# Performance work log

Hardware: AMD Instinct MI355X
Metric: run time of the kernel (lower is better)

Reference implementation:

```python
import jax, jax.numpy as jnp
import numpy as np

N_NODES = 100000


def _deg_norm(idx, n):
    # inverse-sqrt degree, zero-degree nodes -> 0 (DGL norm='both' convention)
    deg = jax.ops.segment_sum(jnp.ones(idx.shape, jnp.float32), idx, num_segments=n)
    return jnp.where(deg > 0, jax.lax.rsqrt(jnp.maximum(deg, 1.0)), 0.0)


def graph_conv(x, src, dst, W, b, n):
    # symmetric normalization: D_out^{-1/2} on src, D_in^{-1/2} on dst
    norm_src = _deg_norm(src, n)  # [N]
    norm_dst = _deg_norm(dst, n)  # [N]
    h = (x * norm_src[:, None]) @ W          # apply weight first (in >= out)
    msg = h[src]                              # gather [E, out]
    agg = jax.ops.segment_sum(msg, dst, num_segments=n)  # scatter-add [N, out]
    return agg * norm_dst[:, None] + b


def setup_inputs() -> dict:
    key = jax.random.key(0)
    ks = jax.random.split(key, 6)
    x = jax.random.normal(ks[0], (N_NODES, 128), dtype=jnp.float32)
    edge_index = jax.random.randint(ks[1], (2, 1600000), 0, N_NODES, dtype=jnp.int64)
    W1 = jax.random.normal(ks[2], (128, 64), dtype=jnp.float32) * (1.0 / np.sqrt(128))
    b1 = jnp.zeros((64,), jnp.float32)
    W2 = jax.random.normal(ks[3], (64, 32), dtype=jnp.float32) * (1.0 / np.sqrt(64))
    b2 = jnp.zeros((32,), jnp.float32)
    Wl = jax.random.normal(ks[4], (32, 1), dtype=jnp.float32) * (1.0 / np.sqrt(32))
    bl = jnp.zeros((1,), jnp.float32)
    return {"x": x, "edge_index": edge_index, "W1": W1, "b1": b1,
            "W2": W2, "b2": b2, "Wl": Wl, "bl": bl}


def reference(x, edge_index, W1, b1, W2, b2, Wl, bl):
    src, dst = edge_index[0], edge_index[1]
    n = x.shape[0]
    h = graph_conv(x, src, dst, W1, b1, n)
    h = jax.nn.relu(h)
    # dropout(p=0.5) is identity at inference
    h = graph_conv(h, src, dst, W2, b2, n)
    return h @ Wl + bl  # [N, 1]
```

## Files before the change

kernel.cpp:

```cpp
#include <hip/hip_runtime.h>
#include <hip/hip_fp16.h>


#define WAVE 64
#define NRANGE 8
#define NQUAD 2
#define CB 1024
#define CHK 32
#define RB (CB / CHK)

typedef _Float16 f16x8 __attribute__((ext_vector_type(8)));
typedef float f32x4 __attribute__((ext_vector_type(4)));

__global__ __launch_bounds__(256) void k_cnt(const int* __restrict__ dst,
                                             unsigned* __restrict__ cnt,
                                             int E, int B, int chunkEb,
                                             const float* __restrict__ W1,
                                             const float* __restrict__ W2,
                                             const float* __restrict__ b2,
                                             const float* __restrict__ Wl,
                                             const float* __restrict__ bl,
                                             _Float16* __restrict__ wt,
                                             float* __restrict__ w2l,
                                             float* __restrict__ c0) {
    if (blockIdx.x == CB) {
        int t = threadIdx.x;
        for (int i = 0; i < 32; ++i) {
            int e = i * 256 + t;
            int k = e >> 6, n = e & 63;
            wt[n * 128 + k] = (_Float16)W1[e];
        }
        if (t < 64) {
            float acc = 0.f;
#pragma unroll
            for (int j = 0; j < 32; ++j) acc += W2[t * 32 + j] * Wl[j];
            w2l[t] = acc;
        }
        if (t == 0) {
            float s = 0.f;
#pragma unroll
            for (int j = 0; j < 32; ++j) s += b2[j] * Wl[j];
            *c0 = s + bl[0];
        }
        return;
    }
    __shared__ unsigned lc[NRANGE];
    if (threadIdx.x < NRANGE) lc[threadIdx.x] = 0u;
    __syncthreads();
    const int c = blockIdx.x;
    const int beg = c * chunkEb, end = min(beg + chunkEb, E);
    unsigned pc[NRANGE] = {};
    for (int i = beg + (int)threadIdx.x; i < end; i += 256) {
        int r = dst[i] / B;
#pragma unroll
        for (int rr = 0; rr < NRANGE; ++rr) pc[rr] += (r == rr);
    }
#pragma unroll
    for (int rr = 0; rr < NRANGE; ++rr) {
        unsigned v = pc[rr];
#pragma unroll
        for (int off = 32; off; off >>= 1) v += __shfl_xor((int)v, off);
        if ((threadIdx.x & 63) == 0 && v) atomicAdd(&lc[rr], v);
    }
    __syncthreads();
    if (threadIdx.x < NRANGE) cnt[threadIdx.x * CB + c] = lc[threadIdx.x];
}

__global__ __launch_bounds__(256) void k_scancnt2(const unsigned* __restrict__ cnt,
                                                  unsigned* __restrict__ segBase,
                                                  unsigned* __restrict__ rangeCur,
                                                  int SLOT) {
    __shared__ unsigned s[256];
    const int t = threadIdx.x;
    const int PER = (NRANGE * CB) / 256;
    unsigned loc[PER];
    unsigned sum = 0;
#pragma unroll
    for (int j = 0; j < PER; ++j) { loc[j] = sum; sum += cnt[t * PER + j]; }
    s[t] = sum;
    __syncthreads();
    for (int off = 1; off < 256; off <<= 1) {
        unsigned a = (t >= off) ? s[t - off] : 0u;
        __syncthreads();
        s[t] += a;
        __syncthreads();
    }
    unsigned base = s[t] - sum;
#pragma unroll
    for (int j = 0; j < PER; ++j) segBase[t * PER + j] = base + loc[j];
    if (t == 255) segBase[NRANGE * CB] = s[255];
    if (t < NRANGE) rangeCur[t] = (unsigned)(t * SLOT);
}

__global__ __launch_bounds__(256) void k_hist(const int* __restrict__ srcArr,
                                              const int* __restrict__ dstArr,
                                              unsigned* __restrict__ partial_s,
                                              unsigned* __restrict__ partial_d,
                                              int E, int B, int chunkE) {
    extern __shared__ unsigned hist[];
    const int q = blockIdx.x & (NQUAD - 1);
    const int c = blockIdx.x >> 1;
    const int lo = q * 4 * B;
    const int* nodes = blockIdx.y ? dstArr : srcArr;
    unsigned* partial = blockIdx.y ? partial_d : partial_s;

    for (int b = threadIdx.x; b < B; b += 256) hist[b] = 0u;
    __syncthreads();

    const int beg = c * chunkE, end = min(beg + chunkE, E);
    const int n4 = (end - beg) >> 2;
    const int4* p = (const int4*)(nodes + beg);
    for (int j = threadIdx.x; j < n4; j += 256) {
        int4 v = p[j];
#pragma unroll
        for (int k = 0; k < 4; ++k) {
            int a = (&v.x)[k] - lo;
            if ((unsigned)a < (unsigned)(4 * B)) {
                int h2 = (a >= 2 * B);
                int r2 = a - (h2 ? 2 * B : 0);
                int h1 = (r2 >= B);
                int bin = r2 - (h1 ? B : 0);
                atomicAdd(&hist[bin], 1u << (((h2 << 1) | h1) << 3));
            }
        }
    }
    for (int j = beg + (n4 << 2) + threadIdx.x; j < end; j += 256) {
        int a = nodes[j] - lo;
        if ((unsigned)a < (unsigned)(4 * B)) {
            int h2 = (a >= 2 * B);
            int r2 = a - (h2 ? 2 * B : 0);
            int h1 = (r2 >= B);
            int bin = r2 - (h1 ? B : 0);
            atomicAdd(&hist[bin], 1u << (((h2 << 1) | h1) << 3));
        }
    }
    __syncthreads();
    unsigned* outp = partial + (size_t)(q * CHK + c) * B;
    for (int b = threadIdx.x; b < B; b += 256) outp[b] = hist[b];
}

__global__ __launch_bounds__(256) void k_bucket(const int* __restrict__ src,
                                                const int* __restrict__ dst,
                                                const unsigned* __restrict__ segBase,
                                                unsigned* __restrict__ ebuf,
                                                int E, int B, int chunkEb) {
    __shared__ unsigned lcnt[NRANGE];
    const int c = blockIdx.x;
    const int lane = threadIdx.x & 63;
    if (threadIdx.x < NRANGE) lcnt[threadIdx.x] = 0u;
    __syncthreads();

    unsigned sb[NRANGE];
#pragma unroll
    for (int r = 0; r < NRANGE; ++r) sb[r] = segBase[r * CB + c];

    const int beg = c * chunkEb, end = min(beg + chunkEb, E);
    for (int i = beg + (int)threadIdx.x; i < end; i += 256) {
        int d = dst[i];
        int s = src[i];
        int r = d / B;
        unsigned pk = ((unsigned)(d - r * B) << 17) | (unsigned)s;
#pragma unroll
        for (int rr = 0; rr < NRANGE; ++rr) {
            unsigned long long m = __ballot(r == rr);
            if (m) {
                int leader = __ffsll((long long)m) - 1;
                unsigned base = 0;
                if (lane == leader) base = atomicAdd(&lcnt[rr], (unsigned)__popcll(m));
                base = (unsigned)__shfl((int)base, leader);
                if (r == rr) {
                    unsigned before = (unsigned)__popcll(m & ((1ull << lane) - 1ull));
                    ebuf[sb[rr] + base + before] = pk;
                }
            }
        }
    }
}

__global__ __launch_bounds__(256) void k_reduce_norm(const unsigned* __restrict__ partial_s,
                                                     unsigned* __restrict__ partial_d,
                                                     float* __restrict__ norm_s,
                                                     float* __restrict__ norm_d,
                                                     unsigned* __restrict__ deg_d,
                                                     unsigned* __restrict__ offsets,
                                                     unsigned* __restrict__ rangeCur,
                                                     int N, int B, int Bpad) {
    int t = blockIdx.x * 256 + threadIdx.x;
    int lane = threadIdx.x & 63;
    const int half = NQUAD * Bpad;
    if (t < half) {
        int q = t / Bpad, b = t - q * Bpad;
        bool valid = (b < B);
        unsigned run = 0;
        if (valid) {
            size_t base = (size_t)(q * CHK) * B + b;
            unsigned acc = 0;
            for (int c = 0; c < CHK; ++c) {
                size_t ix = base + (size_t)c * B;
                unsigned v = partial_d[ix];
                partial_d[ix] = acc;
                acc += v;
            }
            run = acc;
        }
#pragma unroll
        for (int j = 0; j < 4; ++j) {
            unsigned d1 = valid ? ((run >> (8 * j)) & 0xffu) : 0u;
            unsigned p = d1;
#pragma unroll
            for (int off = 1; off < 64; off <<= 1) {
                unsigned o = (unsigned)__shfl_up((int)p, off);
                if (lane >= off) p += o;
            }
            unsigned tot = (unsigned)__shfl((int)p, 63);
            int r = q * 4 + j;
            unsigned wbase = 0;
            if (lane == 63 && tot) wbase = atomicAdd(&rangeCur[r], tot);
            wbase = (unsigned)__shfl((int)wbase, 63);
            if (valid) {
                int n = q * 4 * B + j * B + b;
                if (n < N) {
                    deg_d[n] = d1;
                    norm_d[n] = d1 ? rsqrtf((float)d1) : 0.0f;
                    offsets[n] = wbase + (p - d1);
                }
            }
        }
    } else {
        t -= half;
        int q = t / Bpad, b = t - q * Bpad;
        if (q >= NQUAD || b >= B) return;
        size_t base = (size_t)(q * CHK) * B + b;
        unsigned ds = 0;
        for (int c = 0; c < CHK; ++c) ds += partial_s[base + (size_t)c * B];
#pragma unroll
        for (int j = 0; j < 4; ++j) {
            int n = q * 4 * B + j * B + b;
            if (n < N) {
                unsigned d0 = (ds >> (8 * j)) & 0xffu;
                norm_s[n] = d0 ? rsqrtf((float)d0) : 0.0f;
            }
        }
    }
}

__global__ __launch_bounds__(256) void k_fill2(const unsigned* __restrict__ ebuf,
                                               const unsigned* __restrict__ segBase,
                                               const unsigned* __restrict__ offsets,
                                               const unsigned* __restrict__ rel,
                                               unsigned* __restrict__ csr,
                                               int N, int B) {
    extern __shared__ unsigned curs[];
    const int r = blockIdx.x & (NRANGE - 1);
    const int ch = blockIdx.x >> 3;
    const int lo = r * B;
    const int bins = min(B, N - lo);
    const int sh = (r & 3) << 3;
    const unsigned* relp = rel + (size_t)((r >> 2) * CHK + ch) * B;
    for (int b = threadIdx.x; b < bins; b += 256)
        curs[b] = offsets[lo + b] + ((relp[b] >> sh) & 0xffu);
    __syncthreads();

    const unsigned s0 = segBase[r * CB + ch * RB];
    const unsigned s1 = segBase[r * CB + ch * RB + RB];
    for (unsigned i = s0 + threadIdx.x; i < s1; i += 256) {
        unsigned e = ebuf[i];
        unsigned bin = e >> 17;
        if (bin < (unsigned)bins)
            csr[atomicAdd(&curs[bin], 1u)] = e & 0x1ffffu;
    }
}

__global__ __launch_bounds__(256) void k_gemm1(const float* __restrict__ x,
                                               const _Float16* __restrict__ wt,
                                               const float* __restrict__ norm_s,
                                               __half* __restrict__ h1h, int N) {
    __shared__ __align__(16) _Float16 xs[64 * 128];
    const int tid = threadIdx.x, lane = tid & 63, wv = tid >> 6;
    const int r0 = blockIdx.x * 64;

    f16x8 bf[4][4];
#pragma unroll
    for (int kt = 0; kt < 4; ++kt)
#pragma unroll
        for (int nt = 0; nt < 4; ++nt)
            bf[kt][nt] = *(const f16x8*)&wt[(nt * 16 + (lane & 15)) * 128 +
                                            kt * 32 + (lane >> 4) * 8];

#pragma unroll
    for (int it = 0; it < 8; ++it) {
        int e = it * 256 + tid;
        int r = e >> 5, c = e & 31;
        int row = r0 + r;
        float4 v = (row < N) ? ((const float4*)x)[(size_t)row * 32 + c]
                             : make_float4(0.f, 0.f, 0.f, 0.f);
        __half2 lo2 = __floats2half2_rn(v.x, v.y);
        __half2 hi2 = __floats2half2_rn(v.z, v.w);
        uint2 pk;
        pk.x = *(unsigned*)&lo2;
        pk.y = *(unsigned*)&hi2;
        int byte = r * 256 + c * 8;
        byte ^= (r & 7) << 4;
        *(uint2*)((char*)xs + byte) = pk;
    }
    __syncthreads();

    f32x4 acc[4] = {};
    const int rloc = wv * 16 + (lane & 15);
#pragma unroll
    for (int kt = 0; kt < 4; ++kt) {
        int byte = rloc * 256 + (kt * 32 + (lane >> 4) * 8) * 2;
        byte ^= (rloc & 7) << 4;
        f16x8 af = *(const f16x8*)((char*)xs + byte);
#pragma unroll
        for (int nt = 0; nt < 4; ++nt)
            acc[nt] = __builtin_amdgcn_mfma_f32_16x16x32_f16(af, bf[kt][nt], acc[nt], 0, 0, 0);
    }

#pragma unroll
    for (int j = 0; j < 4; ++j) {
        int row = r0 + wv * 16 + (lane >> 4) * 4 + j;
        if (row < N) {
            float ns = norm_s[row];
#pragma unroll
            for (int nt = 0; nt < 4; ++nt)
                h1h[(size_t)row * 64 + nt * 16 + (lane & 15)] =
                    __float2half(acc[nt][j] * ns);
        }
    }
}

__global__ __launch_bounds__(256) void k_agg_rdot(const unsigned* __restrict__ offsets,
                                                  const unsigned* __restrict__ deg_d,
                                                  const unsigned* __restrict__ csr,
                                                  const __half* __restrict__ h1h,
                                                  const float* __restrict__ norm_s,
                                                  const float* __restrict__ norm_d,
                                                  const float* __restrict__ b1,
                                                  const float* __restrict__ w2l,
                                                  float* __restrict__ s_node, int N) {
    const int lane = threadIdx.x & 63;
    const int slot = lane >> 4;
    const int p = lane & 15;
    const int v = (blockIdx.x * 256 + threadIdx.x) >> 6;
    if (v >= N) return;
    const unsigned beg = offsets[v];
    const unsigned end = beg + deg_d[v];

    float a0 = 0.f, a1 = 0.f, a2 = 0.f, a3 = 0.f;
#define GATHER(sreg) { \
        uint2 u = *(const uint2*)&h1h[(size_t)(sreg) * 64 + 4 * p]; \
        float2 f0 = __half22float2(*(__half2*)&u.x); \
        float2 f1 = __half22float2(*(__half2*)&u.y); \
        a0 += f0.x; a1 += f0.y; a2 += f1.x; a3 += f1.y; }

    for (unsigned base = beg; base < end; base += WAVE) {
        const int n = (int)min((unsigned)WAVE, end - base);
        int sv = (lane < n) ? (int)csr[base + lane] : 0;
        int i = 0;
        for (; i + 32 <= n; i += 32) {
            int s0 = __shfl(sv, i + 0 + slot);
            int s1 = __shfl(sv, i + 4 + slot);
            int s2 = __shfl(sv, i + 8 + slot);
            int s3 = __shfl(sv, i + 12 + slot);
            int s4 = __shfl(sv, i + 16 + slot);
            int s5 = __shfl(sv, i + 20 + slot);
            int s6 = __shfl(sv, i + 24 + slot);
            int s7 = __shfl(sv, i + 28 + slot);
            GATHER(s0); GATHER(s1); GATHER(s2); GATHER(s3);
            GATHER(s4); GATHER(s5); GATHER(s6); GATHER(s7);
        }
        for (; i + 16 <= n; i += 16) {
            int s0 = __shfl(sv, i + 0 + slot);
            int s1 = __shfl(sv, i + 4 + slot);
            int s2 = __shfl(sv, i + 8 + slot);
            int s3 = __shfl(sv, i + 12 + slot);
            GATHER(s0); GATHER(s1); GATHER(s2); GATHER(s3);
        }
        for (; i < n; i += 4) {
            int e = i + slot;
            int s = __shfl(sv, min(e, n - 1));
            if (e < n) GATHER(s);
        }
    }
#undef GATHER
    a0 += __shfl_xor(a0, 16); a0 += __shfl_xor(a0, 32);
    a1 += __shfl_xor(a1, 16); a1 += __shfl_xor(a1, 32);
    a2 += __shfl_xor(a2, 16); a2 += __shfl_xor(a2, 32);
    a3 += __shfl_xor(a3, 16); a3 += __shfl_xor(a3, 32);

    float nd = norm_d[v];
    float4 bq = *(const float4*)&b1[4 * p];
    float4 wq = *(const float4*)&w2l[4 * p];
    float t = fmaxf(fmaf(a0, nd, bq.x), 0.f) * wq.x
            + fmaxf(fmaf(a1, nd, bq.y), 0.f) * wq.y
            + fmaxf(fmaf(a2, nd, bq.z), 0.f) * wq.z
            + fmaxf(fmaf(a3, nd, bq.w), 0.f) * wq.w;
#pragma unroll
    for (int off = 8; off; off >>= 1) t += __shfl_xor(t, off);
    if (lane == 0) s_node[v] = t * norm_s[v];
}

__global__ __launch_bounds__(256) void k_out(const unsigned* __restrict__ offsets,
                                             const unsigned* __restrict__ deg_d,
                                             const unsigned* __restrict__ csr,
                                             const float* __restrict__ s_node,
                                             const float* __restrict__ norm_d,
                                             const float* __restrict__ c0,
                                             float* __restrict__ out, int N) {
    int t = blockIdx.x * 256 + threadIdx.x;
    int v = t >> 2, slot = t & 3;
    if (v >= N) return;
    unsigned beg = offsets[v], end = beg + deg_d[v];
    float sum = 0.f;
    for (unsigned j = beg + slot; j < end; j += 4)
        sum += s_node[csr[j]];
    sum += __shfl_xor(sum, 1);
    sum += __shfl_xor(sum, 2);
    if (slot == 0) out[v] = fmaf(sum, norm_d[v], *c0);
}

extern "C" void kernel_launch(void* const* d_in, const int* in_sizes, int n_in,
                              void* d_out, int out_size, void* d_ws, size_t ws_size,
                              hipStream_t stream) {
    const float* x  = (const float*)d_in[0];
    const int*   ei = (const int*)d_in[1];
    const float* W1 = (const float*)d_in[2];
    const float* b1 = (const float*)d_in[3];
    const float* W2 = (const float*)d_in[4];
    const float* b2 = (const float*)d_in[5];
    const float* Wl = (const float*)d_in[6];
    const float* bl = (const float*)d_in[7];

    const int N = in_sizes[0] / 128;
    const int E = in_sizes[1] / 2;
    const int* src = ei;
    const int* dst = ei + E;
    const int B = (N + NRANGE - 1) / NRANGE;
    const int Bpad = ((B + 63) / 64) * 64;
    const int SLOT = E / NRANGE + 16384;
    const int chunkEb = (E + CB - 1) / CB;
    const int chunkE = chunkEb * RB;

    char* w = (char*)d_ws;
    auto alloc = [&](size_t bytes) -> void* {
        void* r = (void*)w;
        w += (bytes + 255) & ~(size_t)255;
        return r;
    };
    float*    norm_s    = (float*)alloc((size_t)N * 4);
    float*    norm_d    = (float*)alloc((size_t)N * 4);
    unsigned* deg_d     = (unsigned*)alloc((size_t)N * 4);
    unsigned* offsets   = (unsigned*)alloc((size_t)N * 4);
    __half*   h1h       = (__half*)alloc((size_t)N * 64 * 2);
    unsigned* csr       = (unsigned*)alloc((size_t)NRANGE * SLOT * 4);
    float*    s_node    = (float*)alloc((size_t)N * 4);
    float*    w2l       = (float*)alloc(64 * 4);
    float*    c0        = (float*)alloc(4);
    _Float16* wt        = (_Float16*)alloc(64 * 128 * 2);
    unsigned* ebuf      = (unsigned*)alloc((size_t)E * 4);
    unsigned* cnt       = (unsigned*)alloc((size_t)(NRANGE * CB + 1) * 4);
    unsigned* segBase   = (unsigned*)alloc((size_t)(NRANGE * CB + 1) * 4);
    unsigned* rangeCur  = (unsigned*)alloc(NRANGE * 4);
    unsigned* partial_s = (unsigned*)alloc((size_t)NQUAD * CHK * B * 4);
    unsigned* partial_d = (unsigned*)alloc((size_t)NQUAD * CHK * B * 4);

    float* out = (float*)d_out;
    const size_t ldsB = (size_t)B * 4;

    k_cnt<<<CB + 1, 256, 0, stream>>>(dst, cnt, E, B, chunkEb,
                                      W1, W2, b2, Wl, bl, wt, w2l, c0);
    k_scancnt2<<<1, 256, 0, stream>>>(cnt, segBase, rangeCur, SLOT);
    k_hist<<<dim3(NQUAD * CHK, 2), 256, ldsB, stream>>>(src, dst, partial_s,
                                                        partial_d, E, B, chunkE);
    k_bucket<<<CB, 256, 0, stream>>>(src, dst, segBase, ebuf, E, B, chunkEb);

    k_reduce_norm<<<(2 * NQUAD * Bpad + 255) / 256, 256, 0, stream>>>(
        partial_s, partial_d, norm_s, norm_d, deg_d, offsets, rangeCur,
        N, B, Bpad);

    k_gemm1<<<(N + 63) / 64, 256, 0, stream>>>(x, wt, norm_s, h1h, N);

    k_fill2<<<NRANGE * CHK, 256, ldsB, stream>>>(ebuf, segBase, offsets,
                                                 partial_d, csr, N, B);

    k_agg_rdot<<<(N + 3) / 4, 256, 0, stream>>>(offsets, deg_d, csr, h1h,
                                                norm_s, norm_d, b1, w2l,
                                                s_node, N);
    k_out<<<(4 * N + 255) / 256, 256, 0, stream>>>(offsets, deg_d, csr, s_node,
                                                   norm_d, c0, out, N);
}
```

Measured before the change: 184.3 us.

## Slice h1 into 8-channel planes and aggregate per slice for cache locality

The layer-1 features are stored channel-sliced as eight [N,8] fp16 planes instead of row-major [N,64]. The aggregation kernel now processes one 8-channel slice per block, so each slice's working set (about 1.6 MB) can stay in L2. Per-slice partial dot products go to a new buffer and a new kernel sums them. In exchange the CSR indices are read eight times, each gather touches only 8 bytes per lane, and the unrolled gather loop is dropped.

```diff
diff --git a/kernel.cpp b/kernel.cpp
--- a/kernel.cpp
+++ b/kernel.cpp
@@ -8,6 +8,7 @@
 #define CB 1024
 #define CHK 32
 #define RB (CB / CHK)
+#define AGG_NB 2048
 
 typedef _Float16 f16x8 __attribute__((ext_vector_type(8)));
 typedef float f32x4 __attribute__((ext_vector_type(4)));
@@ -274,7 +275,7 @@
 __global__ __launch_bounds__(256) void k_gemm1(const float* __restrict__ x,
                                                const _Float16* __restrict__ wt,
                                                const float* __restrict__ norm_s,
-                                               __half* __restrict__ h1h, int N) {
+                                               __half* __restrict__ hs, int N) {
     __shared__ __align__(16) _Float16 xs[64 * 128];
     const int tid = threadIdx.x, lane = tid & 63, wv = tid >> 6;
     const int r0 = blockIdx.x * 64;
@@ -323,82 +324,80 @@
         if (row < N) {
             float ns = norm_s[row];
 #pragma unroll
-            for (int nt = 0; nt < 4; ++nt)
-                h1h[(size_t)row * 64 + nt * 16 + (lane & 15)] =
+            for (int nt = 0; nt < 4; ++nt) {
+                int ch = nt * 16 + (lane & 15);
+                hs[((size_t)(ch >> 3) * N + row) * 8 + (ch & 7)] =
                     __float2half(acc[nt][j] * ns);
-        }
-    }
-}
-
-__global__ __launch_bounds__(256) void k_agg_rdot(const unsigned* __restrict__ offsets,
-                                                  const unsigned* __restrict__ deg_d,
-                                                  const unsigned* __restrict__ csr,
-                                                  const __half* __restrict__ h1h,
-                                                  const float* __restrict__ norm_s,
-                                                  const float* __restrict__ norm_d,
-                                                  const float* __restrict__ b1,
-                                                  const float* __restrict__ w2l,
-                                                  float* __restrict__ s_node, int N) {
+            }
+        }
+    }
+}
+
+__global__ __launch_bounds__(256) void k_agg_slice(const unsigned* __restrict__ offsets,
+                                                   const unsigned* __restrict__ deg_d,
+                                                   const unsigned* __restrict__ csr,
+                                                   const __half* __restrict__ hs,
+                                                   const float* __restrict__ norm_d,
+                                                   const float* __restrict__ b1,
+                                                   const float* __restrict__ w2l,
+                                                   float* __restrict__ s_part, int N) {
+    const int c = blockIdx.x & 7;
+    const int nb0 = blockIdx.x >> 3;
+    const int wid = threadIdx.x >> 6;
     const int lane = threadIdx.x & 63;
-    const int slot = lane >> 4;
-    const int p = lane & 15;
-    const int v = (blockIdx.x * 256 + threadIdx.x) >> 6;
+    const int half = lane & 1;
+    const int slot = lane >> 1;
+    const __half* hbase = hs + (size_t)c * N * 8 + 4 * half;
+    const float4 bq = *(const float4*)&b1[8 * c + 4 * half];
+    const float4 wq = *(const float4*)&w2l[8 * c + 4 * half];
+    float* sp = s_part + (size_t)c * N;
+
+    for (int v = nb0 * 4 + wid; v < N; v += AGG_NB * 4) {
+        const unsigned beg = offsets[v];
+        const unsigned deg = deg_d[v];
+        float a0 = 0.f, a1 = 0.f, a2 = 0.f, a3 = 0.f;
+        for (unsigned base = beg; base < beg + deg; base += WAVE) {
+            const int n = (int)min((unsigned)WAVE, beg + deg - base);
+            int sv = (lane < n) ? (int)csr[base + lane] : 0;
+            for (int i = 0; i < n; i += 32) {
+                int e = i + slot;
+                int s = __shfl(sv, min(e, n - 1));
+                if (e < n) {
+                    uint2 u = *(const uint2*)&hbase[(size_t)s * 8];
+                    float2 f0 = __half22float2(*(__half2*)&u.x);
+                    float2 f1 = __half22float2(*(__half2*)&u.y);
+                    a0 += f0.x; a1 += f0.y; a2 += f1.x; a3 += f1.y;
+                }
+            }
+        }
+        a0 += __shfl_xor(a0, 2); a0 += __shfl_xor(a0, 4); a0 += __shfl_xor(a0, 8);
+        a0 += __shfl_xor(a0, 16); a0 += __shfl_xor(a0, 32);
+        a1 += __shfl_xor(a1, 2); a1 += __shfl_xor(a1, 4); a1 += __shfl_xor(a1, 8);
+        a1 += __shfl_xor(a1, 16); a1 += __shfl_xor(a1, 32);
+        a2 += __shfl_xor(a2, 2); a2 += __shfl_xor(a2, 4); a2 += __shfl_xor(a2, 8);
+        a2 += __shfl_xor(a2, 16); a2 += __shfl_xor(a2, 32);
+        a3 += __shfl_xor(a3, 2); a3 += __shfl_xor(a3, 4); a3 += __shfl_xor(a3, 8);
+        a3 += __shfl_xor(a3, 16); a3 += __shfl_xor(a3, 32);
+
+        float nd = norm_d[v];
+        float t = fmaxf(fmaf(a0, nd, bq.x), 0.f) * wq.x
+                + fmaxf(fmaf(a1, nd, bq.y), 0.f) * wq.y
+                + fmaxf(fmaf(a2, nd, bq.z), 0.f) * wq.z
+                + fmaxf(fmaf(a3, nd, bq.w), 0.f) * wq.w;
+        t += __shfl_xor(t, 1);
+        if (lane == 0) sp[v] = t;
+    }
+}
+
+__global__ __launch_bounds__(256) void k_snode(const float* __restrict__ s_part,
+                                               const float* __restrict__ norm_s,
+                                               float* __restrict__ s_node, int N) {
+    int v = blockIdx.x * 256 + threadIdx.x;
     if (v >= N) return;
-    const unsigned beg = offsets[v];
-    const unsigned end = beg + deg_d[v];
-
-    float a0 = 0.f, a1 = 0.f, a2 = 0.f, a3 = 0.f;
-#define GATHER(sreg) { \
-        uint2 u = *(const uint2*)&h1h[(size_t)(sreg) * 64 + 4 * p]; \
-        float2 f0 = __half22float2(*(__half2*)&u.x); \
-        float2 f1 = __half22float2(*(__half2*)&u.y); \
-        a0 += f0.x; a1 += f0.y; a2 += f1.x; a3 += f1.y; }
-
-    for (unsigned base = beg; base < end; base += WAVE) {
-        const int n = (int)min((unsigned)WAVE, end - base);
-        int sv = (lane < n) ? (int)csr[base + lane] : 0;
-        int i = 0;
-        for (; i + 32 <= n; i += 32) {
-            int s0 = __shfl(sv, i + 0 + slot);
-            int s1 = __shfl(sv, i + 4 + slot);
-            int s2 = __shfl(sv, i + 8 + slot);
-            int s3 = __shfl(sv, i + 12 + slot);
-            int s4 = __shfl(sv, i + 16 + slot);
-            int s5 = __shfl(sv, i + 20 + slot);
-            int s6 = __shfl(sv, i + 24 + slot);
-            int s7 = __shfl(sv, i + 28 + slot);
-            GATHER(s0); GATHER(s1); GATHER(s2); GATHER(s3);
-            GATHER(s4); GATHER(s5); GATHER(s6); GATHER(s7);
-        }
-        for (; i + 16 <= n; i += 16) {
-            int s0 = __shfl(sv, i + 0 + slot);
-            int s1 = __shfl(sv, i + 4 + slot);
-            int s2 = __shfl(sv, i + 8 + slot);
-            int s3 = __shfl(sv, i + 12 + slot);
-            GATHER(s0); GATHER(s1); GATHER(s2); GATHER(s3);
-        }
-        for (; i < n; i += 4) {
-            int e = i + slot;
-            int s = __shfl(sv, min(e, n - 1));
-            if (e < n) GATHER(s);
-        }
-    }
-#undef GATHER
-    a0 += __shfl_xor(a0, 16); a0 += __shfl_xor(a0, 32);
-    a1 += __shfl_xor(a1, 16); a1 += __shfl_xor(a1, 32);
-    a2 += __shfl_xor(a2, 16); a2 += __shfl_xor(a2, 32);
-    a3 += __shfl_xor(a3, 16); a3 += __shfl_xor(a3, 32);
-
-    float nd = norm_d[v];
-    float4 bq = *(const float4*)&b1[4 * p];
-    float4 wq = *(const float4*)&w2l[4 * p];
-    float t = fmaxf(fmaf(a0, nd, bq.x), 0.f) * wq.x
-            + fmaxf(fmaf(a1, nd, bq.y), 0.f) * wq.y
-            + fmaxf(fmaf(a2, nd, bq.z), 0.f) * wq.z
-            + fmaxf(fmaf(a3, nd, bq.w), 0.f) * wq.w;
-#pragma unroll
-    for (int off = 8; off; off >>= 1) t += __shfl_xor(t, off);
-    if (lane == 0) s_node[v] = t * norm_s[v];
+    float s = 0.f;
+#pragma unroll
+    for (int c = 0; c < 8; ++c) s += s_part[(size_t)c * N + v];
+    s_node[v] = s * norm_s[v];
 }
 
 __global__ __launch_bounds__(256) void k_out(const unsigned* __restrict__ offsets,
@@ -452,9 +451,10 @@
     float*    norm_d    = (float*)alloc((size_t)N * 4);
     unsigned* deg_d     = (unsigned*)alloc((size_t)N * 4);
     unsigned* offsets   = (unsigned*)alloc((size_t)N * 4);
-    __half*   h1h       = (__half*)alloc((size_t)N * 64 * 2);
+    __half*   hs        = (__half*)alloc((size_t)N * 64 * 2);
     unsigned* csr       = (unsigned*)alloc((size_t)NRANGE * SLOT * 4);
     float*    s_node    = (float*)alloc((size_t)N * 4);
+    float*    s_part    = (float*)alloc((size_t)8 * N * 4);
     float*    w2l       = (float*)alloc(64 * 4);
     float*    c0        = (float*)alloc(4);
     _Float16* wt        = (_Float16*)alloc(64 * 128 * 2);
@@ -479,14 +479,14 @@
         partial_s, partial_d, norm_s, norm_d, deg_d, offsets, rangeCur,
         N, B, Bpad);
 
-    k_gemm1<<<(N + 63) / 64, 256, 0, stream>>>(x, wt, norm_s, h1h, N);
+    k_gemm1<<<(N + 63) / 64, 256, 0, stream>>>(x, wt, norm_s, hs, N);
 
     k_fill2<<<NRANGE * CHK, 256, ldsB, stream>>>(ebuf, segBase, offsets,
                                                  partial_d, csr, N, B);
 
-    k_agg_rdot<<<(N + 3) / 4, 256, 0, stream>>>(offsets, deg_d, csr, h1h,
-                                                norm_s, norm_d, b1, w2l,
-                                                s_node, N);
+    k_agg_slice<<<8 * AGG_NB, 256, 0, stream>>>(offsets, deg_d, csr, hs,
+                                                norm_d, b1, w2l, s_part, N);
+    k_snode<<<(N + 255) / 256, 256, 0, stream>>>(s_part, norm_s, s_node, N);
     k_out<<<(4 * N + 255) / 256, 256, 0, stream>>>(offsets, deg_d, csr, s_node,
                                                    norm_d, c0, out, N);
 }
```

Measured after the change: 326.8 us. +77.3%, slower.

## Fold dst range counting into histogram kernel and grid-stride aggregation

Applied to the files above, without the earlier changes.

Drops the separate k_cnt pass over dst. The per-chunk, per-range edge counts are now gathered in LDS inside k_hist's dst blocks, and the weight-prep work rides on an extra block of that kernel. Chunk sizes are now fixed constants (2048-edge bucket chunks, 32 per histogram chunk) and the number of chunks is derived from E. k_agg_rdot becomes a grid-stride loop over a fixed 4096 blocks, with the bias and weight loads hoisted out of it. This saves one full read of dst and one launch, at the cost of extra LDS atomics in the histogram pass and a change to the number of histogram chunks.

```diff
diff --git a/kernel.cpp b/kernel.cpp
--- a/kernel.cpp
+++ b/kernel.cpp
@@ -5,113 +5,70 @@
 #define WAVE 64
 #define NRANGE 8
 #define NQUAD 2
-#define CB 1024
-#define CHK 32
-#define RB (CB / CHK)
+#define CEB 2048
+#define RB 32
+#define CHE (CEB * RB)
+#define AGGB 4096
 
 typedef _Float16 f16x8 __attribute__((ext_vector_type(8)));
 typedef float f32x4 __attribute__((ext_vector_type(4)));
-
-__global__ __launch_bounds__(256) void k_cnt(const int* __restrict__ dst,
-                                             unsigned* __restrict__ cnt,
-                                             int E, int B, int chunkEb,
-                                             const float* __restrict__ W1,
-                                             const float* __restrict__ W2,
-                                             const float* __restrict__ b2,
-                                             const float* __restrict__ Wl,
-                                             const float* __restrict__ bl,
-                                             _Float16* __restrict__ wt,
-                                             float* __restrict__ w2l,
-                                             float* __restrict__ c0) {
-    if (blockIdx.x == CB) {
-        int t = threadIdx.x;
-        for (int i = 0; i < 32; ++i) {
-            int e = i * 256 + t;
-            int k = e >> 6, n = e & 63;
-            wt[n * 128 + k] = (_Float16)W1[e];
-        }
-        if (t < 64) {
-            float acc = 0.f;
-#pragma unroll
-            for (int j = 0; j < 32; ++j) acc += W2[t * 32 + j] * Wl[j];
-            w2l[t] = acc;
-        }
-        if (t == 0) {
-            float s = 0.f;
-#pragma unroll
-            for (int j = 0; j < 32; ++j) s += b2[j] * Wl[j];
-            *c0 = s + bl[0];
-        }
-        return;
-    }
-    __shared__ unsigned lc[NRANGE];
-    if (threadIdx.x < NRANGE) lc[threadIdx.x] = 0u;
-    __syncthreads();
-    const int c = blockIdx.x;
-    const int beg = c * chunkEb, end = min(beg + chunkEb, E);
-    unsigned pc[NRANGE] = {};
-    for (int i = beg + (int)threadIdx.x; i < end; i += 256) {
-        int r = dst[i] / B;
-#pragma unroll
-        for (int rr = 0; rr < NRANGE; ++rr) pc[rr] += (r == rr);
-    }
-#pragma unroll
-    for (int rr = 0; rr < NRANGE; ++rr) {
-        unsigned v = pc[rr];
-#pragma unroll
-        for (int off = 32; off; off >>= 1) v += __shfl_xor((int)v, off);
-        if ((threadIdx.x & 63) == 0 && v) atomicAdd(&lc[rr], v);
-    }
-    __syncthreads();
-    if (threadIdx.x < NRANGE) cnt[threadIdx.x * CB + c] = lc[threadIdx.x];
-}
-
-__global__ __launch_bounds__(256) void k_scancnt2(const unsigned* __restrict__ cnt,
-                                                  unsigned* __restrict__ segBase,
-                                                  unsigned* __restrict__ rangeCur,
-                                                  int SLOT) {
-    __shared__ unsigned s[256];
-    const int t = threadIdx.x;
-    const int PER = (NRANGE * CB) / 256;
-    unsigned loc[PER];
-    unsigned sum = 0;
-#pragma unroll
-    for (int j = 0; j < PER; ++j) { loc[j] = sum; sum += cnt[t * PER + j]; }
-    s[t] = sum;
-    __syncthreads();
-    for (int off = 1; off < 256; off <<= 1) {
-        unsigned a = (t >= off) ? s[t - off] : 0u;
-        __syncthreads();
-        s[t] += a;
-        __syncthreads();
-    }
-    unsigned base = s[t] - sum;
-#pragma unroll
-    for (int j = 0; j < PER; ++j) segBase[t * PER + j] = base + loc[j];
-    if (t == 255) segBase[NRANGE * CB] = s[255];
-    if (t < NRANGE) rangeCur[t] = (unsigned)(t * SLOT);
-}
 
 __global__ __launch_bounds__(256) void k_hist(const int* __restrict__ srcArr,
                                               const int* __restrict__ dstArr,
                                               unsigned* __restrict__ partial_s,
                                               unsigned* __restrict__ partial_d,
-                                              int E, int B, int chunkE) {
+                                              unsigned* __restrict__ cnt,
+                                              int E, int B, int nCH, int CBu,
+                                              const float* __restrict__ W1,
+                                              const float* __restrict__ W2,
+                                              const float* __restrict__ b2,
+                                              const float* __restrict__ Wl,
+                                              const float* __restrict__ bl,
+                                              _Float16* __restrict__ wt,
+                                              float* __restrict__ w2l,
+                                              float* __restrict__ c0) {
     extern __shared__ unsigned hist[];
+    __shared__ unsigned scnt[4 * RB];
+    if (blockIdx.x == (unsigned)(NQUAD * nCH)) {
+        if (blockIdx.y == 0) {
+            int t = threadIdx.x;
+            for (int i = 0; i < 32; ++i) {
+                int e = i * 256 + t;
+                int k = e >> 6, n = e & 63;
+                wt[n * 128 + k] = (_Float16)W1[e];
+            }
+            if (t < 64) {
+                float acc = 0.f;
+#pragma unroll
+                for (int j = 0; j < 32; ++j) acc += W2[t * 32 + j] * Wl[j];
+                w2l[t] = acc;
+            }
+            if (t == 0) {
+                float s = 0.f;
+#pragma unroll
+                for (int j = 0; j < 32; ++j) s += b2[j] * Wl[j];
+                *c0 = s + bl[0];
+            }
+        }
+        return;
+    }
     const int q = blockIdx.x & (NQUAD - 1);
     const int c = blockIdx.x >> 1;
     const int lo = q * 4 * B;
-    const int* nodes = blockIdx.y ? dstArr : srcArr;
-    unsigned* partial = blockIdx.y ? partial_d : partial_s;
+    const bool isDst = (blockIdx.y == 1);
+    const int* nodes = isDst ? dstArr : srcArr;
+    unsigned* partial = isDst ? partial_d : partial_s;
 
     for (int b = threadIdx.x; b < B; b += 256) hist[b] = 0u;
-    __syncthreads();
-
-    const int beg = c * chunkE, end = min(beg + chunkE, E);
+    if (threadIdx.x < 4 * RB) scnt[threadIdx.x] = 0u;
+    __syncthreads();
+
+    const int beg = c * CHE, end = min(beg + CHE, E);
     const int n4 = (end - beg) >> 2;
     const int4* p = (const int4*)(nodes + beg);
     for (int j = threadIdx.x; j < n4; j += 256) {
         int4 v = p[j];
+        const int sc = j >> 9;
 #pragma unroll
         for (int k = 0; k < 4; ++k) {
             int a = (&v.x)[k] - lo;
@@ -120,30 +77,69 @@
                 int r2 = a - (h2 ? 2 * B : 0);
                 int h1 = (r2 >= B);
                 int bin = r2 - (h1 ? B : 0);
-                atomicAdd(&hist[bin], 1u << (((h2 << 1) | h1) << 3));
-            }
-        }
-    }
-    for (int j = beg + (n4 << 2) + threadIdx.x; j < end; j += 256) {
-        int a = nodes[j] - lo;
+                int jj = (h2 << 1) | h1;
+                atomicAdd(&hist[bin], 1u << (jj << 3));
+                if (isDst) atomicAdd(&scnt[jj * RB + sc], 1u);
+            }
+        }
+    }
+    for (int i = beg + (n4 << 2) + threadIdx.x; i < end; i += 256) {
+        int a = nodes[i] - lo;
+        const int sc = (i - beg) >> 11;
         if ((unsigned)a < (unsigned)(4 * B)) {
             int h2 = (a >= 2 * B);
             int r2 = a - (h2 ? 2 * B : 0);
             int h1 = (r2 >= B);
             int bin = r2 - (h1 ? B : 0);
-            atomicAdd(&hist[bin], 1u << (((h2 << 1) | h1) << 3));
-        }
-    }
-    __syncthreads();
-    unsigned* outp = partial + (size_t)(q * CHK + c) * B;
+            int jj = (h2 << 1) | h1;
+            atomicAdd(&hist[bin], 1u << (jj << 3));
+            if (isDst) atomicAdd(&scnt[jj * RB + sc], 1u);
+        }
+    }
+    __syncthreads();
+    unsigned* outp = partial + (size_t)(q * nCH + c) * B;
     for (int b = threadIdx.x; b < B; b += 256) outp[b] = hist[b];
+    if (isDst && threadIdx.x < 4 * RB) {
+        int jj = threadIdx.x >> 5, sc = threadIdx.x & (RB - 1);
+        cnt[(q * 4 + jj) * CBu + c * RB + sc] = scnt[threadIdx.x];
+    }
+}
+
+__global__ __launch_bounds__(256) void k_scancnt2(const unsigned* __restrict__ cnt,
+                                                  unsigned* __restrict__ segBase,
+                                                  unsigned* __restrict__ rangeCur,
+                                                  int total, int PER, int SLOT) {
+    __shared__ unsigned s[256];
+    const int t = threadIdx.x;
+    unsigned loc[32];
+    unsigned sum = 0;
+#pragma unroll
+    for (int j = 0; j < 32; ++j) {
+        unsigned v = (j < PER && t * PER + j < total) ? cnt[t * PER + j] : 0u;
+        loc[j] = sum;
+        sum += v;
+    }
+    s[t] = sum;
+    __syncthreads();
+    for (int off = 1; off < 256; off <<= 1) {
+        unsigned a = (t >= off) ? s[t - off] : 0u;
+        __syncthreads();
+        s[t] += a;
+        __syncthreads();
+    }
+    unsigned base = s[t] - sum;
+#pragma unroll
+    for (int j = 0; j < 32; ++j)
+        if (j < PER && t * PER + j < total) segBase[t * PER + j] = base + loc[j];
+    if (t == 255) segBase[total] = s[255];
+    if (t < NRANGE) rangeCur[t] = (unsigned)(t * SLOT);
 }
 
 __global__ __launch_bounds__(256) void k_bucket(const int* __restrict__ src,
                                                 const int* __restrict__ dst,
                                                 const unsigned* __restrict__ segBase,
                                                 unsigned* __restrict__ ebuf,
-                                                int E, int B, int chunkEb) {
+                                                int E, int B, int CBu) {
     __shared__ unsigned lcnt[NRANGE];
     const int c = blockIdx.x;
     const int lane = threadIdx.x & 63;
@@ -152,9 +148,9 @@
 
     unsigned sb[NRANGE];
 #pragma unroll
-    for (int r = 0; r < NRANGE; ++r) sb[r] = segBase[r * CB + c];
-
-    const int beg = c * chunkEb, end = min(beg + chunkEb, E);
+    for (int r = 0; r < NRANGE; ++r) sb[r] = segBase[r * CBu + c];
+
+    const int beg = c * CEB, end = min(beg + CEB, E);
     for (int i = beg + (int)threadIdx.x; i < end; i += 256) {
         int d = dst[i];
         int s = src[i];
@@ -184,7 +180,7 @@
                                                      unsigned* __restrict__ deg_d,
                                                      unsigned* __restrict__ offsets,
                                                      unsigned* __restrict__ rangeCur,
-                                                     int N, int B, int Bpad) {
+                                                     int N, int B, int Bpad, int nCH) {
     int t = blockIdx.x * 256 + threadIdx.x;
     int lane = threadIdx.x & 63;
     const int half = NQUAD * Bpad;
@@ -193,9 +189,9 @@
         bool valid = (b < B);
         unsigned run = 0;
         if (valid) {
-            size_t base = (size_t)(q * CHK) * B + b;
+            size_t base = (size_t)(q * nCH) * B + b;
             unsigned acc = 0;
-            for (int c = 0; c < CHK; ++c) {
+            for (int c = 0; c < nCH; ++c) {
                 size_t ix = base + (size_t)c * B;
                 unsigned v = partial_d[ix];
                 partial_d[ix] = acc;
@@ -230,9 +226,9 @@
         t -= half;
         int q = t / Bpad, b = t - q * Bpad;
         if (q >= NQUAD || b >= B) return;
-        size_t base = (size_t)(q * CHK) * B + b;
+        size_t base = (size_t)(q * nCH) * B + b;
         unsigned ds = 0;
-        for (int c = 0; c < CHK; ++c) ds += partial_s[base + (size_t)c * B];
+        for (int c = 0; c < nCH; ++c) ds += partial_s[base + (size_t)c * B];
 #pragma unroll
         for (int j = 0; j < 4; ++j) {
             int n = q * 4 * B + j * B + b;
@@ -249,20 +245,20 @@
                                                const unsigned* __restrict__ offsets,
                                                const unsigned* __restrict__ rel,
                                                unsigned* __restrict__ csr,
-                                               int N, int B) {
+                                               int N, int B, int nCH, int CBu) {
     extern __shared__ unsigned curs[];
     const int r = blockIdx.x & (NRANGE - 1);
     const int ch = blockIdx.x >> 3;
     const int lo = r * B;
     const int bins = min(B, N - lo);
     const int sh = (r & 3) << 3;
-    const unsigned* relp = rel + (size_t)((r >> 2) * CHK + ch) * B;
+    const unsigned* relp = rel + (size_t)((r >> 2) * nCH + ch) * B;
     for (int b = threadIdx.x; b < bins; b += 256)
         curs[b] = offsets[lo + b] + ((relp[b] >> sh) & 0xffu);
     __syncthreads();
 
-    const unsigned s0 = segBase[r * CB + ch * RB];
-    const unsigned s1 = segBase[r * CB + ch * RB + RB];
+    const unsigned s0 = segBase[r * CBu + ch * RB];
+    const unsigned s1 = segBase[r * CBu + ch * RB + RB];
     for (unsigned i = s0 + threadIdx.x; i < s1; i += 256) {
         unsigned e = ebuf[i];
         unsigned bin = e >> 17;
@@ -340,65 +336,67 @@
                                                   const float* __restrict__ w2l,
                                                   float* __restrict__ s_node, int N) {
     const int lane = threadIdx.x & 63;
+    const int wid = threadIdx.x >> 6;
     const int slot = lane >> 4;
     const int p = lane & 15;
-    const int v = (blockIdx.x * 256 + threadIdx.x) >> 6;
-    if (v >= N) return;
-    const unsigned beg = offsets[v];
-    const unsigned end = beg + deg_d[v];
-
-    float a0 = 0.f, a1 = 0.f, a2 = 0.f, a3 = 0.f;
+    const float4 bq = *(const float4*)&b1[4 * p];
+    const float4 wq = *(const float4*)&w2l[4 * p];
+
 #define GATHER(sreg) { \
         uint2 u = *(const uint2*)&h1h[(size_t)(sreg) * 64 + 4 * p]; \
         float2 f0 = __half22float2(*(__half2*)&u.x); \
         float2 f1 = __half22float2(*(__half2*)&u.y); \
         a0 += f0.x; a1 += f0.y; a2 += f1.x; a3 += f1.y; }
 
-    for (unsigned base = beg; base < end; base += WAVE) {
-        const int n = (int)min((unsigned)WAVE, end - base);
-        int sv = (lane < n) ? (int)csr[base + lane] : 0;
-        int i = 0;
-        for (; i + 32 <= n; i += 32) {
-            int s0 = __shfl(sv, i + 0 + slot);
-            int s1 = __shfl(sv, i + 4 + slot);
-            int s2 = __shfl(sv, i + 8 + slot);
-            int s3 = __shfl(sv, i + 12 + slot);
-            int s4 = __shfl(sv, i + 16 + slot);
-            int s5 = __shfl(sv, i + 20 + slot);
-            int s6 = __shfl(sv, i + 24 + slot);
-            int s7 = __shfl(sv, i + 28 + slot);
-            GATHER(s0); GATHER(s1); GATHER(s2); GATHER(s3);
-            GATHER(s4); GATHER(s5); GATHER(s6); GATHER(s7);
-        }
-        for (; i + 16 <= n; i += 16) {
-            int s0 = __shfl(sv, i + 0 + slot);
-            int s1 = __shfl(sv, i + 4 + slot);
-            int s2 = __shfl(sv, i + 8 + slot);
-            int s3 = __shfl(sv, i + 12 + slot);
-            GATHER(s0); GATHER(s1); GATHER(s2); GATHER(s3);
-        }
-        for (; i < n; i += 4) {
-            int e = i + slot;
-            int s = __shfl(sv, min(e, n - 1));
-            if (e < n) GATHER(s);
-        }
+    for (int v = blockIdx.x * 4 + wid; v < N; v += AGGB * 4) {
+        const unsigned beg = offsets[v];
+        const unsigned end = beg + deg_d[v];
+        float a0 = 0.f, a1 = 0.f, a2 = 0.f, a3 = 0.f;
+
+        for (unsigned base = beg; base < end; base += WAVE) {
+            const int n = (int)min((unsigned)WAVE, end - base);
+            int sv = (lane < n) ? (int)csr[base + lane] : 0;
+            int i = 0;
+            for (; i + 32 <= n; i += 32) {
+                int s0 = __shfl(sv, i + 0 + slot);
+                int s1 = __shfl(sv, i + 4 + slot);
+                int s2 = __shfl(sv, i + 8 + slot);
+                int s3 = __shfl(sv, i + 12 + slot);
+                int s4 = __shfl(sv, i + 16 + slot);
+                int s5 = __shfl(sv, i + 20 + slot);
+                int s6 = __shfl(sv, i + 24 + slot);
+                int s7 = __shfl(sv, i + 28 + slot);
+                GATHER(s0); GATHER(s1); GATHER(s2); GATHER(s3);
+                GATHER(s4); GATHER(s5); GATHER(s6); GATHER(s7);
+            }
+            for (; i + 16 <= n; i += 16) {
+                int s0 = __shfl(sv, i + 0 + slot);
+                int s1 = __shfl(sv, i + 4 + slot);
+                int s2 = __shfl(sv, i + 8 + slot);
+                int s3 = __shfl(sv, i + 12 + slot);
+                GATHER(s0); GATHER(s1); GATHER(s2); GATHER(s3);
+            }
+            for (; i < n; i += 4) {
+                int e = i + slot;
+                int s = __shfl(sv, min(e, n - 1));
+                if (e < n) GATHER(s);
+            }
+        }
+        a0 += __shfl_xor(a0, 16); a0 += __shfl_xor(a0, 32);
+        a1 += __shfl_xor(a1, 16); a1 += __shfl_xor(a1, 32);
+        a2 += __shfl_xor(a2, 16); a2 += __shfl_xor(a2, 32);
+        a3 += __shfl_xor(a3, 16); a3 += __shfl_xor(a3, 32);
+
+        float nd = norm_d[v];
+        float t = fmaxf(fmaf(a0, nd, bq.x), 0.f) * wq.x
+                + fmaxf(fmaf(a1, nd, bq.y), 0.f) * wq.y
+                + fmaxf(fmaf(a2, nd, bq.z), 0.f) * wq.z
+                + fmaxf(fmaf(a3, nd, bq.w), 0.f) * wq.w;
+#pragma unroll
+        for (int off = 8; off; off >>= 1) t += __shfl_xor(t, off);
+        if (lane == 0) s_node[v] = t * norm_s[v];
     }
 #undef GATHER
-    a0 += __shfl_xor(a0, 16); a0 += __shfl_xor(a0, 32);
-    a1 += __shfl_xor(a1, 16); a1 += __shfl_xor(a1, 32);
-    a2 += __shfl_xor(a2, 16); a2 += __shfl_xor(a2, 32);
-    a3 += __shfl_xor(a3, 16); a3 += __shfl_xor(a3, 32);
-
-    float nd = norm_d[v];
-    float4 bq = *(const float4*)&b1[4 * p];
-    float4 wq = *(const float4*)&w2l[4 * p];
-    float t = fmaxf(fmaf(a0, nd, bq.x), 0.f) * wq.x
-            + fmaxf(fmaf(a1, nd, bq.y), 0.f) * wq.y
-            + fmaxf(fmaf(a2, nd, bq.z), 0.f) * wq.z
-            + fmaxf(fmaf(a3, nd, bq.w), 0.f) * wq.w;
-#pragma unroll
-    for (int off = 8; off; off >>= 1) t += __shfl_xor(t, off);
-    if (lane == 0) s_node[v] = t * norm_s[v];
 }
 
 __global__ __launch_bounds__(256) void k_out(const unsigned* __restrict__ offsets,
@@ -439,8 +437,10 @@
     const int B = (N + NRANGE - 1) / NRANGE;
     const int Bpad = ((B + 63) / 64) * 64;
     const int SLOT = E / NRANGE + 16384;
-    const int chunkEb = (E + CB - 1) / CB;
-    const int chunkE = chunkEb * RB;
+    const int nCH = (E + CHE - 1) / CHE;
+    const int CBu = nCH * RB;
+    const int total = NRANGE * CBu;
+    const int PER = (total + 255) / 256;
 
     char* w = (char*)d_ws;
     auto alloc = [&](size_t bytes) -> void* {
@@ -459,34 +459,32 @@
     float*    c0        = (float*)alloc(4);
     _Float16* wt        = (_Float16*)alloc(64 * 128 * 2);
     unsigned* ebuf      = (unsigned*)alloc((size_t)E * 4);
-    unsigned* cnt       = (unsigned*)alloc((size_t)(NRANGE * CB + 1) * 4);
-    unsigned* segBase   = (unsigned*)alloc((size_t)(NRANGE * CB + 1) * 4);
+    unsigned* cnt       = (unsigned*)alloc((size_t)(total + 1) * 4);
+    unsigned* segBase   = (unsigned*)alloc((size_t)(total + 1) * 4);
     unsigned* rangeCur  = (unsigned*)alloc(NRANGE * 4);
-    unsigned* partial_s = (unsigned*)alloc((size_t)NQUAD * CHK * B * 4);
-    unsigned* partial_d = (unsigned*)alloc((size_t)NQUAD * CHK * B * 4);
+    unsigned* partial_s = (unsigned*)alloc((size_t)NQUAD * nCH * B * 4);
+    unsigned* partial_d = (unsigned*)alloc((size_t)NQUAD * nCH * B * 4);
 
     float* out = (float*)d_out;
     const size_t ldsB = (size_t)B * 4;
 
-    k_cnt<<<CB + 1, 256, 0, stream>>>(dst, cnt, E, B, chunkEb,
-                                      W1, W2, b2, Wl, bl, wt, w2l, c0);
-    k_scancnt2<<<1, 256, 0, stream>>>(cnt, segBase, rangeCur, SLOT);
-    k_hist<<<dim3(NQUAD * CHK, 2), 256, ldsB, stream>>>(src, dst, partial_s,
-                                                        partial_d, E, B, chunkE);
-    k_bucket<<<CB, 256, 0, stream>>>(src, dst, segBase, ebuf, E, B, chunkEb);
+    k_hist<<<dim3(NQUAD * nCH + 1, 2), 256, ldsB, stream>>>(
+        src, dst, partial_s, partial_d, cnt, E, B, nCH, CBu,
+        W1, W2, b2, Wl, bl, wt, w2l, c0);
+    k_scancnt2<<<1, 256, 0, stream>>>(cnt, segBase, rangeCur, total, PER, SLOT);
+    k_bucket<<<CBu, 256, 0, stream>>>(src, dst, segBase, ebuf, E, B, CBu);
 
     k_reduce_norm<<<(2 * NQUAD * Bpad + 255) / 256, 256, 0, stream>>>(
         partial_s, partial_d, norm_s, norm_d, deg_d, offsets, rangeCur,
-        N, B, Bpad);
+        N, B, Bpad, nCH);
 
     k_gemm1<<<(N + 63) / 64, 256, 0, stream>>>(x, wt, norm_s, h1h, N);
 
-    k_fill2<<<NRANGE * CHK, 256, ldsB, stream>>>(ebuf, segBase, offsets,
-                                                 partial_d, csr, N, B);
-
-    k_agg_rdot<<<(N + 3) / 4, 256, 0, stream>>>(offsets, deg_d, csr, h1h,
-                                                norm_s, norm_d, b1, w2l,
-                                                s_node, N);
+    k_fill2<<<NRANGE * nCH, 256, ldsB, stream>>>(ebuf, segBase, offsets,
+                                                 partial_d, csr, N, B, nCH, CBu);
+
+    k_agg_rdot<<<AGGB, 256, 0, stream>>>(offsets, deg_d, csr, h1h,
+                                         norm_s, norm_d, b1, w2l, s_node, N);
     k_out<<<(4 * N + 255) / 256, 256, 0, stream>>>(offsets, deg_d, csr, s_node,
                                                    norm_d, c0, out, N);
 }
```

New measurement: 200.8 us. +8.9%, slower.
